# Kernel tuning notes

Hardware: AMD Instinct MI355X
Metric: run time of the kernel (lower is better)

Reference implementation:

```python
import jax, jax.numpy as jnp
import numpy as np

DN = ('NCHW', 'OIHW', 'NCHW')

def _conv(x, w, padding):
    return jax.lax.conv_general_dilated(
        x, w, window_strides=(1, 1), padding=padding,
        dimension_numbers=DN)

def setup_inputs() -> dict:
    key = jax.random.key(0)
    k1, k2, k3, k4, k5 = jax.random.split(key, 5)
    nf = 40
    x = jax.random.normal(k1, (16, nf, 256, 256), dtype=jnp.float32)
    # PyTorch conv default init scale ~ 1/sqrt(fan_in)
    w2 = jax.random.normal(k2, (nf, nf, 1, 1), dtype=jnp.float32) / np.sqrt(nf)
    b2 = jax.random.normal(k3, (nf,), dtype=jnp.float32) * 0.01
    w3 = jax.random.normal(k4, (nf, nf, 3, 3), dtype=jnp.float32) / np.sqrt(nf * 9)
    w4 = jax.random.normal(k5, (nf, nf, 3, 3), dtype=jnp.float32) / np.sqrt(nf * 9)
    return {"x": x, "w2": w2, "b2": b2, "w3": w3, "w4": w4}

def reference(x, w2, b2, w3, w4):
    # k2: 1x1 conv + bias, then sigmoid gate (pixel attention)
    y = _conv(x, w2, padding='VALID') + b2[None, :, None, None]
    y = jax.nn.sigmoid(y)
    # k3: 3x3 conv (pad 1, no bias), gated elementwise
    out = _conv(x, w3, padding=((1, 1), (1, 1))) * y
    # k4: 3x3 conv (pad 1, no bias)
    out = _conv(out, w4, padding=((1, 1), (1, 1)))
    return out
```

## Files before the change

kernel.cpp:

```cpp
#include <hip/hip_runtime.h>
#include <hip/hip_bf16.h>

typedef __bf16 bf16;
typedef __bf16 bf16x2 __attribute__((ext_vector_type(2)));
typedef __bf16 bf16x4 __attribute__((ext_vector_type(4)));
typedef __bf16 bf16x8 __attribute__((ext_vector_type(8)));
typedef float f32x4 __attribute__((ext_vector_type(4)));

#define NF 40
#define HW 256
#define KPAD 384
#define MPAD 48

#define ZROW_ELEM_OFF (2 * MPAD * KPAD + MPAD * 64)
#define GATED_ELEM_OFF 40960
#define IMG_ELEMS ((size_t)16 * HW * HW * NF)
#define XT_ELEM_OFF (GATED_ELEM_OFF + IMG_ELEMS)
#define WS_FULL  ((GATED_ELEM_OFF + 2 * IMG_ELEMS) * 2)

#define PLANE ((size_t)HW * HW * 8)
#define IMGSTR ((size_t)HW * HW * NF)

#define SRW 34
#define SRH 10
#define SRU 340
#define SGS 2720
#define SNU 1700
#define SBUF 14336

__device__ __forceinline__ void gload_lds16(const bf16* g, bf16* l) {
  __builtin_amdgcn_global_load_lds(
      (const __attribute__((address_space(1))) void*)g,
      (__attribute__((address_space(3))) void*)l, 16, 0, 0);
}

__global__ void prep_weights(const float* __restrict__ w2,
                             const float* __restrict__ w3,
                             const float* __restrict__ w4,
                             bf16* __restrict__ ws) {
  int i = blockIdx.x * 256 + threadIdx.x;
  const int T = MPAD * KPAD;
  if (i < T) {
    int co = i / KPAD, k = i % KPAD;
    float v3 = 0.f, v4 = 0.f;
    if (co < NF && k < 360) {
      int tap = k / NF, ci = k - tap * NF;
      int ky = tap / 3, kx = tap - ky * 3;
      int idx = ((co * NF + ci) * 3 + ky) * 3 + kx;
      v3 = w3[idx];
      v4 = w4[idx];
    }
    ws[i] = (bf16)v3;
    ws[T + i] = (bf16)v4;
  }
  if (i < MPAD * 64) {
    int co = i / 64, ci = i - co * 64;
    float v = 0.f;
    if (co < NF && ci < NF) v = w2[co * NF + ci];
    ws[2 * T + i] = (bf16)v;
  }
  if (i < 1024) ws[ZROW_ELEM_OFF + i] = (bf16)0.f;
}

__global__ __launch_bounds__(256, 8)
void transpose_nhwc(const float* __restrict__ x, bf16* __restrict__ xT) {
  __shared__ bf16 xs[5 * 2056];
  const int tid = threadIdx.x;
  const int row = blockIdx.x;
  const int n   = blockIdx.y;
  const size_t nb = (size_t)n * NF * HW * HW + (size_t)row * HW;

#pragma unroll
  for (int cc = 0; cc < 10; ++cc) {
    bf16x4 v;
#pragma unroll
    for (int j = 0; j < 4; ++j)
      v[j] = (bf16)x[nb + (size_t)(cc * 4 + j) * HW * HW + tid];
    *(bf16x4*)&xs[(cc >> 1) * 2056 + tid * 8 + (cc & 1) * 4] = v;
  }
  __syncthreads();

  const size_t ob = ((size_t)n * HW * HW + (size_t)row * HW) * NF;
#pragma unroll
  for (int k = 0; k < 10; ++k) {
    int u = tid + k * 256;
    int px = u / 10, c4 = u - px * 10;
    bf16x4 v = *(const bf16x4*)&xs[(c4 >> 1) * 2056 + px * 8 + (c4 & 1) * 4];
    *(bf16x4*)&xT[ob + (size_t)u * 4] = v;
  }
}

__global__ __launch_bounds__(256, 2)
void k1_sweep(const bf16* __restrict__ xT, const float* __restrict__ b2,
              const bf16* __restrict__ ws, bf16* __restrict__ gated) {
  __shared__ bf16 xs[2][SBUF];

  const int tid  = threadIdx.x;
  const int lane = tid & 63;
  const int wid  = tid >> 6;
  const int l15  = lane & 15;
  const int lk   = lane >> 4;
  const int n    = blockIdx.z;
  const int X0   = blockIdx.x * 32;
  const int Yb   = blockIdx.y * 64;

  const bf16* W3A  = ws;
  const bf16* W2A  = ws + 2 * MPAD * KPAD;
  const bf16* zrow = ws + ZROW_ELEM_OFF;
  const bf16* bn   = xT + (size_t)n * IMGSTR;

  int gp3[12];
#pragma unroll
  for (int kk = 0; kk < 12; ++kk) {
    int k0 = kk * 32 + lk * 8;
    int kc = (k0 < 360) ? k0 : 0;
    int tap = kc / NF, ci0 = kc - tap * NF;
    int ky = tap / 3, kx = tap - ky * 3;
    gp3[kk] = (ci0 >> 3) * SGS + (ky * SRW + kx) * 8;
  }
  int gctr[2];
#pragma unroll
  for (int kk = 0; kk < 2; ++kk) {
    int k0 = kk * 32 + lk * 8;
    int ci0 = (k0 < NF) ? k0 : 0;
    gctr[kk] = (ci0 >> 3) * SGS + (SRW + 1) * 8;
  }
  int pb[4];
#pragma unroll
  for (int q = 0; q < 4; ++q) {
    int prow = wid * 2 + (q >> 1);
    int pcol = (q & 1) * 16 + l15;
    pb[q] = (prow * SRW + pcol) * 8;
  }
  float b2v[3][4];
#pragma unroll
  for (int mt = 0; mt < 3; ++mt)
#pragma unroll
    for (int r = 0; r < 4; ++r) {
      int co = mt * 16 + lk * 4 + r;
      b2v[mt][r] = (co < NF) ? b2[co] : 0.f;
    }
  bf16x8 a2[2][3];
#pragma unroll
  for (int kk = 0; kk < 2; ++kk)
#pragma unroll
    for (int mt = 0; mt < 3; ++mt)
      a2[kk][mt] = *(const bf16x8*)&W2A[(mt * 16 + l15) * 64 + kk * 32 + lk * 8];

  int uc8[7], ur[7], ugx[7], uld[7];
  bool uok[7];
#pragma unroll
  for (int it = 0; it < 7; ++it) {
    int u0 = it * 256 + wid * 64;
    int u  = u0 + lane;
    int c   = u / SRU;
    int rem = u - c * SRU;
    int r   = rem / SRW;
    int p   = rem - r * SRW;
    int gx  = X0 - 1 + p;
    uok[it] = (u < SNU) && ((unsigned)gx < HW);
    uc8[it] = (c << 3);
    ur[it]  = r;
    ugx[it] = ((unsigned)gx < HW) ? gx : 0;
    uld[it] = u0 * 8;
  }

  {
    int ys = Yb - 1;
#pragma unroll
    for (int it = 0; it < 7; ++it) {
      int gy = ys + ur[it];
      bool ok = uok[it] && ((unsigned)gy < HW);
      const bf16* src = ok ? (bn + (size_t)(gy * HW + ugx[it]) * NF + uc8[it]) : zrow;
      gload_lds16(src, &xs[0][uld[it]]);
    }
  }
  __syncthreads();

  for (int s = 0; s < 8; ++s) {
    const bf16* buf = xs[s & 1];

    if (s < 7) {
      int ys = Yb + (s + 1) * 8 - 1;
      bf16* nbuf = xs[(s & 1) ^ 1];
#pragma unroll
      for (int it = 0; it < 7; ++it) {
        int gy = ys + ur[it];
        bool ok = uok[it] && ((unsigned)gy < HW);
        const bf16* src = ok ? (bn + (size_t)(gy * HW + ugx[it]) * NF + uc8[it]) : zrow;
        gload_lds16(src, &nbuf[uld[it]]);
      }
    }

    bf16x4 gv[4][3];
    {
      f32x4 g[4][3];
#pragma unroll
      for (int q = 0; q < 4; ++q)
#pragma unroll
        for (int mt = 0; mt < 3; ++mt) g[q][mt] = f32x4{0, 0, 0, 0};
#pragma unroll
      for (int kk = 0; kk < 2; ++kk)
#pragma unroll
        for (int q = 0; q < 4; ++q) {
          bf16x8 b = *(const bf16x8*)&buf[gctr[kk] + pb[q]];
#pragma unroll
          for (int mt = 0; mt < 3; ++mt)
            g[q][mt] = __builtin_amdgcn_mfma_f32_16x16x32_bf16(a2[kk][mt], b, g[q][mt], 0, 0, 0);
        }
#pragma unroll
      for (int q = 0; q < 4; ++q)
#pragma unroll
        for (int mt = 0; mt < 3; ++mt)
#pragma unroll
          for (int r = 0; r < 4; ++r)
            gv[q][mt][r] = (bf16)(1.f / (1.f + __expf(-(g[q][mt][r] + b2v[mt][r]))));
    }

    f32x4 f[4][3];
#pragma unroll
    for (int q = 0; q < 4; ++q)
#pragma unroll
      for (int mt = 0; mt < 3; ++mt) f[q][mt] = f32x4{0, 0, 0, 0};

#pragma unroll
    for (int kk = 0; kk < 12; ++kk) {
      bf16x8 a[3];
#pragma unroll
      for (int mt = 0; mt < 3; ++mt)
        a[mt] = *(const bf16x8*)&W3A[(mt * 16 + l15) * KPAD + kk * 32 + lk * 8];
#pragma unroll
      for (int q = 0; q < 4; ++q) {
        bf16x8 b = *(const bf16x8*)&buf[gp3[kk] + pb[q]];
#pragma unroll
        for (int mt = 0; mt < 3; ++mt)
          f[q][mt] = __builtin_amdgcn_mfma_f32_16x16x32_bf16(a[mt], b, f[q][mt], 0, 0, 0);
      }
    }

#pragma unroll
    for (int q = 0; q < 4; ++q) {
      int prow = wid * 2 + (q >> 1);
      int pcol = (q & 1) * 16 + l15;
      size_t pix8 = ((size_t)(Yb + s * 8 + prow) * HW + (X0 + pcol)) * 8;
#pragma unroll
      for (int mt = 0; mt < 3; ++mt) {
        int co0 = mt * 16 + lk * 4;
        if (co0 < NF) {
          int cg = co0 >> 3;
          bf16x4 ov;
#pragma unroll
          for (int r = 0; r < 4; ++r)
            ov[r] = (bf16)(f[q][mt][r] * (float)gv[q][mt][r]);
          *(bf16x4*)&gated[(size_t)n * IMGSTR + (size_t)cg * PLANE + pix8 + (co0 & 7)] = ov;
        }
      }
    }

    __syncthreads();
  }
}

__global__ __launch_bounds__(256, 2)
void k2_sweep(const bf16* __restrict__ gated, const bf16* __restrict__ ws,
              float* __restrict__ out) {
  __shared__ bf16 xs[2][SBUF];

  const int tid  = threadIdx.x;
  const int lane = tid & 63;
  const int wid  = tid >> 6;
  const int l15  = lane & 15;
  const int lk   = lane >> 4;
  const int n    = blockIdx.z;
  const int X0   = blockIdx.x * 32;
  const int Yb   = blockIdx.y * 64;

  const bf16* W4A  = ws + MPAD * KPAD;
  const bf16* zrow = ws + ZROW_ELEM_OFF;
  const bf16* bn   = gated + (size_t)n * IMGSTR;

  int gp4[12];
#pragma unroll
  for (int kk = 0; kk < 12; ++kk) {
    int k0 = kk * 32 + lk * 8;
    int kc = (k0 < 360) ? k0 : 0;
    int tap = kc / NF, ci0 = kc - tap * NF;
    int ky = tap / 3, kx = tap - ky * 3;
    gp4[kk] = (ci0 >> 3) * SGS + (ky * SRW + kx) * 8;
  }
  int pb[4];
#pragma unroll
  for (int q = 0; q < 4; ++q) {
    int prow = wid * 2 + (q >> 1);
    int pcol = (q & 1) * 16 + l15;
    pb[q] = (prow * SRW + pcol) * 8;
  }

  int ucp[7], ur[7], ugx[7], uld[7];
  bool uok[7];
#pragma unroll
  for (int it = 0; it < 7; ++it) {
    int u0 = it * 256 + wid * 64;
    int u  = u0 + lane;
    int c   = u / SRU;
    int rem = u - c * SRU;
    int r   = rem / SRW;
    int p   = rem - r * SRW;
    int gx  = X0 - 1 + p;
    uok[it] = (u < SNU) && ((unsigned)gx < HW);
    ucp[it] = (c < 5) ? c : 0;
    ur[it]  = r;
    ugx[it] = ((unsigned)gx < HW) ? gx : 0;
    uld[it] = u0 * 8;
  }

  {
    int ys = Yb - 1;
#pragma unroll
    for (int it = 0; it < 7; ++it) {
      int gy = ys + ur[it];
      bool ok = uok[it] && ((unsigned)gy < HW);
      const bf16* src = ok ? (bn + (size_t)ucp[it] * PLANE + (size_t)(gy * HW + ugx[it]) * 8) : zrow;
      gload_lds16(src, &xs[0][uld[it]]);
    }
  }
  __syncthreads();

  float* on = out + (size_t)n * NF * HW * HW;

  for (int s = 0; s < 8; ++s) {
    const bf16* buf = xs[s & 1];

    if (s < 7) {
      int ys = Yb + (s + 1) * 8 - 1;
      bf16* nbuf = xs[(s & 1) ^ 1];
#pragma unroll
      for (int it = 0; it < 7; ++it) {
        int gy = ys + ur[it];
        bool ok = uok[it] && ((unsigned)gy < HW);
        const bf16* src = ok ? (bn + (size_t)ucp[it] * PLANE + (size_t)(gy * HW + ugx[it]) * 8) : zrow;
        gload_lds16(src, &nbuf[uld[it]]);
      }
    }

    f32x4 f[4][3];
#pragma unroll
    for (int q = 0; q < 4; ++q)
#pragma unroll
      for (int mt = 0; mt < 3; ++mt) f[q][mt] = f32x4{0, 0, 0, 0};

#pragma unroll
    for (int kk = 0; kk < 12; ++kk) {
      bf16x8 a[3];
#pragma unroll
      for (int mt = 0; mt < 3; ++mt)
        a[mt] = *(const bf16x8*)&W4A[(mt * 16 + l15) * KPAD + kk * 32 + lk * 8];
#pragma unroll
      for (int q = 0; q < 4; ++q) {
        bf16x8 b = *(const bf16x8*)&buf[gp4[kk] + pb[q]];
#pragma unroll
        for (int mt = 0; mt < 3; ++mt)
          f[q][mt] = __builtin_amdgcn_mfma_f32_16x16x32_bf16(a[mt], b, f[q][mt], 0, 0, 0);
      }
    }

#pragma unroll
    for (int q = 0; q < 4; ++q) {
      int prow = wid * 2 + (q >> 1);
      int pcol = (q & 1) * 16 + l15;
      float* orow = on + (size_t)(Yb + s * 8 + prow) * HW + (X0 + pcol);
#pragma unroll
      for (int mt = 0; mt < 3; ++mt)
#pragma unroll
        for (int r = 0; r < 4; ++r) {
          int co = mt * 16 + lk * 4 + r;
          if (co < NF)
            orow[(size_t)co * HW * HW] = f[q][mt][r];
        }
    }

    __syncthreads();
  }
}

#define K1_RW 18
__global__ __launch_bounds__(512, 6)
void k1_gate_nchw(const float* __restrict__ x, const float* __restrict__ b2,
                  const bf16* __restrict__ ws, bf16* __restrict__ gated) {
  __shared__ bf16 xs[K1_RW * K1_RW * NF];

  const int tid  = threadIdx.x;
  const int lane = tid & 63;
  const int wid  = tid >> 6;
  const int l15  = lane & 15;
  const int lk   = lane >> 4;
  const int n    = blockIdx.z;
  const int X0   = blockIdx.x * 16;
  const int Y0   = blockIdx.y * 16;

  const bf16* W3A = ws;
  const bf16* W2A = ws + 2 * MPAD * KPAD;

  const float* xn = x + (size_t)n * NF * HW * HW;
  for (int i = tid; i < K1_RW * K1_RW * NF / 2; i += 512) {
    int cih = i / (K1_RW * K1_RW);
    int rem = i - cih * (K1_RW * K1_RW);
    int ci  = cih * 2;
    int yy  = rem / K1_RW, xx = rem - yy * K1_RW;
    int gy  = Y0 - 1 + yy, gx = X0 - 1 + xx;
    float v0 = 0.f, v1 = 0.f;
    if ((unsigned)gy < HW && (unsigned)gx < HW) {
      const float* p = xn + (size_t)ci * HW * HW + gy * HW + gx;
      v0 = p[0];
      v1 = p[HW * HW];
    }
    bf16x2 pr; pr[0] = (bf16)v0; pr[1] = (bf16)v1;
    *(bf16x2*)&xs[rem * NF + ci] = pr;
  }

  int off3[12];
#pragma unroll
  for (int kk = 0; kk < 12; ++kk) {
    int k0 = kk * 32 + lk * 8;
    int kc = (k0 < 360) ? k0 : 0;
    int tap = kc / NF, ci0 = kc - tap * NF;
    int ky = tap / 3, kx = tap - ky * 3;
    off3[kk] = (ky * K1_RW + kx) * NF + ci0;
  }
  int pb[2];
#pragma unroll
  for (int t2 = 0; t2 < 2; ++t2) {
    int pix = (wid * 2 + t2) * 16 + l15;
    int py = pix >> 4, px = pix & 15;
    pb[t2] = (py * K1_RW + px) * NF;
  }
  float b2v[3][4];
#pragma unroll
  for (int mt = 0; mt < 3; ++mt)
#pragma unroll
    for (int r = 0; r < 4; ++r) {
      int co = mt * 16 + lk * 4 + r;
      b2v[mt][r] = (co < NF) ? b2[co] : 0.f;
    }

  __syncthreads();

  bf16x4 gv[2][3];
  {
    f32x4 g[2][3];
#pragma unroll
    for (int t2 = 0; t2 < 2; ++t2)
#pragma unroll
      for (int mt = 0; mt < 3; ++mt) g[t2][mt] = f32x4{0, 0, 0, 0};
#pragma unroll
    for (int kk = 0; kk < 2; ++kk) {
      int k0 = kk * 32 + lk * 8;
      int goff = (K1_RW + 1) * NF + ((k0 < NF) ? k0 : 0);
      bf16x8 a[3];
#pragma unroll
      for (int mt = 0; mt < 3; ++mt)
        a[mt] = *(const bf16x8*)&W2A[(mt * 16 + l15) * 64 + k0];
#pragma unroll
      for (int t2 = 0; t2 < 2; ++t2) {
        bf16x8 b = *(const bf16x8*)&xs[pb[t2] + goff];
#pragma unroll
        for (int mt = 0; mt < 3; ++mt)
          g[t2][mt] = __builtin_amdgcn_mfma_f32_16x16x32_bf16(a[mt], b, g[t2][mt], 0, 0, 0);
      }
    }
#pragma unroll
    for (int t2 = 0; t2 < 2; ++t2)
#pragma unroll
      for (int mt = 0; mt < 3; ++mt)
#pragma unroll
        for (int r = 0; r < 4; ++r)
          gv[t2][mt][r] = (bf16)(1.f / (1.f + __expf(-(g[t2][mt][r] + b2v[mt][r]))));
  }

  f32x4 facc[2][3];
#pragma unroll
  for (int t2 = 0; t2 < 2; ++t2)
#pragma unroll
    for (int mt = 0; mt < 3; ++mt) facc[t2][mt] = f32x4{0, 0, 0, 0};

#pragma unroll
  for (int kk = 0; kk < 12; ++kk) {
    bf16x8 a[3];
#pragma unroll
    for (int mt = 0; mt < 3; ++mt)
      a[mt] = *(const bf16x8*)&W3A[(mt * 16 + l15) * KPAD + kk * 32 + lk * 8];
#pragma unroll
    for (int t2 = 0; t2 < 2; ++t2) {
      bf16x8 b = *(const bf16x8*)&xs[pb[t2] + off3[kk]];
#pragma unroll
      for (int mt = 0; mt < 3; ++mt)
        facc[t2][mt] = __builtin_amdgcn_mfma_f32_16x16x32_bf16(a[mt], b, facc[t2][mt], 0, 0, 0);
    }
  }

#pragma unroll
  for (int t2 = 0; t2 < 2; ++t2) {
    int pix = (wid * 2 + t2) * 16 + l15;
    int py = pix >> 4, px = pix & 15;
    size_t pix8 = ((size_t)(Y0 + py) * HW + (X0 + px)) * 8;
#pragma unroll
    for (int mt = 0; mt < 3; ++mt) {
      int co0 = mt * 16 + lk * 4;
      if (co0 < NF) {
        int cg = co0 >> 3;
        bf16x4 ov;
#pragma unroll
        for (int r = 0; r < 4; ++r)
          ov[r] = (bf16)(facc[t2][mt][r] * (float)gv[t2][mt][r]);
        *(bf16x4*)&gated[(size_t)n * IMGSTR + (size_t)cg * PLANE + pix8 + (co0 & 7)] = ov;
      }
    }
  }
}

extern "C" void kernel_launch(void* const* d_in, const int* in_sizes, int n_in,
                              void* d_out, int out_size, void* d_ws, size_t ws_size,
                              hipStream_t stream) {
  const float* x  = (const float*)d_in[0];
  const float* w2 = (const float*)d_in[1];
  const float* b2 = (const float*)d_in[2];
  const float* w3 = (const float*)d_in[3];
  const float* w4 = (const float*)d_in[4];
  float* out = (float*)d_out;
  bf16* ws   = (bf16*)d_ws;

  hipLaunchKernelGGL(prep_weights, dim3(72), dim3(256), 0, stream, w2, w3, w4, ws);

  bf16* gated = ws + GATED_ELEM_OFF;
  if (ws_size >= WS_FULL) {
    bf16* xT = ws + XT_ELEM_OFF;
    hipLaunchKernelGGL(transpose_nhwc, dim3(256, 16), dim3(256), 0, stream, x, xT);
    hipLaunchKernelGGL(k1_sweep, dim3(8, 4, 16), dim3(256), 0, stream,
                       xT, b2, ws, gated);
  } else {
    hipLaunchKernelGGL(k1_gate_nchw, dim3(16, 16, 16), dim3(512), 0, stream,
                       x, b2, ws, gated);
  }
  hipLaunchKernelGGL(k2_sweep, dim3(8, 4, 16), dim3(256), 0, stream,
                     gated, ws, out);
}
```

Baseline: 285.4 us.

## Relax per-step barriers to partial vmcnt waits, precompute load pointers, raise MFMA priority

Both sweep kernels end each row step with an explicit s_waitcnt vmcnt(N) plus s_barrier instead of __syncthreads. The intent is that the prefetch loads into LDS must finish, but the global stores just issued can stay in flight. The per-iteration prefetch address math is replaced by pointers computed once and advanced by a fixed stride, with a special case for the bottom boundary tile. The MFMA loops are wrapped in s_setprio to favour the compute waves. Correctness now depends on the counted number of stores per thread and on in-order vmcnt accounting.

```diff
diff --git a/kernel.cpp b/kernel.cpp
--- a/kernel.cpp
+++ b/kernel.cpp
@@ -22,7 +22,6 @@
 #define IMGSTR ((size_t)HW * HW * NF)
 
 #define SRW 34
-#define SRH 10
 #define SRU 340
 #define SGS 2720
 #define SNU 1700
@@ -33,6 +32,9 @@
       (const __attribute__((address_space(1))) void*)g,
       (__attribute__((address_space(3))) void*)l, 16, 0, 0);
 }
+
+#define BARRIER_VM(N)                                                        \
+  asm volatile("s_waitcnt vmcnt(" #N ") lgkmcnt(0)\n\ts_barrier" ::: "memory")
 
 __global__ void prep_weights(const float* __restrict__ w2,
                              const float* __restrict__ w3,
@@ -103,6 +105,7 @@
   const int n    = blockIdx.z;
   const int X0   = blockIdx.x * 32;
   const int Yb   = blockIdx.y * 64;
+  const bool lasty = (Yb == HW - 64);
 
   const bf16* W3A  = ws;
   const bf16* W2A  = ws + 2 * MPAD * KPAD;
@@ -127,11 +130,8 @@
   }
   int pb[4];
 #pragma unroll
-  for (int q = 0; q < 4; ++q) {
-    int prow = wid * 2 + (q >> 1);
-    int pcol = (q & 1) * 16 + l15;
-    pb[q] = (prow * SRW + pcol) * 8;
-  }
+  for (int q = 0; q < 4; ++q)
+    pb[q] = ((wid * 2 + (q >> 1)) * SRW + (q & 1) * 16 + l15) * 8;
   float b2v[3][4];
 #pragma unroll
   for (int mt = 0; mt < 3; ++mt)
@@ -147,7 +147,7 @@
     for (int mt = 0; mt < 3; ++mt)
       a2[kk][mt] = *(const bf16x8*)&W2A[(mt * 16 + l15) * 64 + kk * 32 + lk * 8];
 
-  int uc8[7], ur[7], ugx[7], uld[7];
+  int ur[7], ugx[7], uc8[7], uld[7];
   bool uok[7];
 #pragma unroll
   for (int it = 0; it < 7; ++it) {
@@ -159,11 +159,18 @@
     int p   = rem - r * SRW;
     int gx  = X0 - 1 + p;
     uok[it] = (u < SNU) && ((unsigned)gx < HW);
-    uc8[it] = (c << 3);
     ur[it]  = r;
     ugx[it] = ((unsigned)gx < HW) ? gx : 0;
+    uc8[it] = (c << 3);
     uld[it] = u0 * 8;
   }
+
+  const bf16* P[7];
+#pragma unroll
+  for (int it = 0; it < 7; ++it)
+    P[it] = uok[it] ? (bn + (size_t)((Yb + 7 + ur[it]) * HW + ugx[it]) * NF + uc8[it])
+                    : zrow;
+  const size_t PSTEP = (size_t)8 * HW * NF;
 
   {
     int ys = Yb - 1;
@@ -175,22 +182,32 @@
       gload_lds16(src, &xs[0][uld[it]]);
     }
   }
-  __syncthreads();
+  asm volatile("s_waitcnt vmcnt(0) lgkmcnt(0)\n\ts_barrier" ::: "memory");
+
+  bf16* gbase = gated + (size_t)n * IMGSTR;
+  size_t e0 = ((size_t)(Yb + wid * 2) * HW + X0 + l15) * 8;
+  const size_t ESTEP = (size_t)8 * HW * 8;
 
   for (int s = 0; s < 8; ++s) {
     const bf16* buf = xs[s & 1];
 
     if (s < 7) {
-      int ys = Yb + (s + 1) * 8 - 1;
       bf16* nbuf = xs[(s & 1) ^ 1];
-#pragma unroll
-      for (int it = 0; it < 7; ++it) {
-        int gy = ys + ur[it];
-        bool ok = uok[it] && ((unsigned)gy < HW);
-        const bf16* src = ok ? (bn + (size_t)(gy * HW + ugx[it]) * NF + uc8[it]) : zrow;
-        gload_lds16(src, &nbuf[uld[it]]);
-      }
-    }
+      if (lasty && s == 6) {
+#pragma unroll
+        for (int it = 0; it < 7; ++it) {
+          bool ok = uok[it] && (ur[it] < 9);
+          gload_lds16(ok ? P[it] : zrow, &nbuf[uld[it]]);
+        }
+      } else {
+#pragma unroll
+        for (int it = 0; it < 7; ++it) {
+          gload_lds16(P[it], &nbuf[uld[it]]);
+          P[it] += uok[it] ? PSTEP : 0;
+        }
+      }
+    }
+    asm volatile("" ::: "memory");
 
     bf16x4 gv[4][3];
     {
@@ -223,6 +240,7 @@
 #pragma unroll
       for (int mt = 0; mt < 3; ++mt) f[q][mt] = f32x4{0, 0, 0, 0};
 
+    __builtin_amdgcn_s_setprio(1);
 #pragma unroll
     for (int kk = 0; kk < 12; ++kk) {
       bf16x8 a[3];
@@ -237,12 +255,11 @@
           f[q][mt] = __builtin_amdgcn_mfma_f32_16x16x32_bf16(a[mt], b, f[q][mt], 0, 0, 0);
       }
     }
+    __builtin_amdgcn_s_setprio(0);
 
 #pragma unroll
     for (int q = 0; q < 4; ++q) {
-      int prow = wid * 2 + (q >> 1);
-      int pcol = (q & 1) * 16 + l15;
-      size_t pix8 = ((size_t)(Yb + s * 8 + prow) * HW + (X0 + pcol)) * 8;
+      size_t pix8 = e0 + (size_t)(((q >> 1) * HW + (q & 1) * 16) * 8);
 #pragma unroll
       for (int mt = 0; mt < 3; ++mt) {
         int co0 = mt * 16 + lk * 4;
@@ -252,12 +269,13 @@
 #pragma unroll
           for (int r = 0; r < 4; ++r)
             ov[r] = (bf16)(f[q][mt][r] * (float)gv[q][mt][r]);
-          *(bf16x4*)&gated[(size_t)n * IMGSTR + (size_t)cg * PLANE + pix8 + (co0 & 7)] = ov;
-        }
-      }
-    }
-
-    __syncthreads();
+          *(bf16x4*)&gbase[(size_t)cg * PLANE + pix8 + (co0 & 7)] = ov;
+        }
+      }
+    }
+    e0 += ESTEP;
+
+    BARRIER_VM(8);
   }
 }
 
@@ -274,6 +292,7 @@
   const int n    = blockIdx.z;
   const int X0   = blockIdx.x * 32;
   const int Yb   = blockIdx.y * 64;
+  const bool lasty = (Yb == HW - 64);
 
   const bf16* W4A  = ws + MPAD * KPAD;
   const bf16* zrow = ws + ZROW_ELEM_OFF;
@@ -290,13 +309,10 @@
   }
   int pb[4];
 #pragma unroll
-  for (int q = 0; q < 4; ++q) {
-    int prow = wid * 2 + (q >> 1);
-    int pcol = (q & 1) * 16 + l15;
-    pb[q] = (prow * SRW + pcol) * 8;
-  }
-
-  int ucp[7], ur[7], ugx[7], uld[7];
+  for (int q = 0; q < 4; ++q)
+    pb[q] = ((wid * 2 + (q >> 1)) * SRW + (q & 1) * 16 + l15) * 8;
+
+  int ur[7], ugx[7], ucp[7], uld[7];
   bool uok[7];
 #pragma unroll
   for (int it = 0; it < 7; ++it) {
@@ -308,11 +324,19 @@
     int p   = rem - r * SRW;
     int gx  = X0 - 1 + p;
     uok[it] = (u < SNU) && ((unsigned)gx < HW);
-    ucp[it] = (c < 5) ? c : 0;
     ur[it]  = r;
     ugx[it] = ((unsigned)gx < HW) ? gx : 0;
+    ucp[it] = (c < 5) ? c : 0;
     uld[it] = u0 * 8;
   }
+
+  const bf16* P[7];
+#pragma unroll
+  for (int it = 0; it < 7; ++it)
+    P[it] = uok[it] ? (bn + (size_t)ucp[it] * PLANE +
+                       (size_t)((Yb + 7 + ur[it]) * HW + ugx[it]) * 8)
+                    : zrow;
+  const size_t PSTEP = (size_t)8 * HW * 8;
 
   {
     int ys = Yb - 1;
@@ -320,28 +344,37 @@
     for (int it = 0; it < 7; ++it) {
       int gy = ys + ur[it];
       bool ok = uok[it] && ((unsigned)gy < HW);
-      const bf16* src = ok ? (bn + (size_t)ucp[it] * PLANE + (size_t)(gy * HW + ugx[it]) * 8) : zrow;
+      const bf16* src = ok ? (bn + (size_t)ucp[it] * PLANE + (size_t)(gy * HW + ugx[it]) * 8)
+                           : zrow;
       gload_lds16(src, &xs[0][uld[it]]);
     }
   }
-  __syncthreads();
+  asm volatile("s_waitcnt vmcnt(0) lgkmcnt(0)\n\ts_barrier" ::: "memory");
 
   float* on = out + (size_t)n * NF * HW * HW;
+  size_t o0 = (size_t)(Yb + wid * 2) * HW + X0 + l15;
+  const size_t OSTEP = (size_t)8 * HW;
 
   for (int s = 0; s < 8; ++s) {
     const bf16* buf = xs[s & 1];
 
     if (s < 7) {
-      int ys = Yb + (s + 1) * 8 - 1;
       bf16* nbuf = xs[(s & 1) ^ 1];
-#pragma unroll
-      for (int it = 0; it < 7; ++it) {
-        int gy = ys + ur[it];
-        bool ok = uok[it] && ((unsigned)gy < HW);
-        const bf16* src = ok ? (bn + (size_t)ucp[it] * PLANE + (size_t)(gy * HW + ugx[it]) * 8) : zrow;
-        gload_lds16(src, &nbuf[uld[it]]);
-      }
-    }
+      if (lasty && s == 6) {
+#pragma unroll
+        for (int it = 0; it < 7; ++it) {
+          bool ok = uok[it] && (ur[it] < 9);
+          gload_lds16(ok ? P[it] : zrow, &nbuf[uld[it]]);
+        }
+      } else {
+#pragma unroll
+        for (int it = 0; it < 7; ++it) {
+          gload_lds16(P[it], &nbuf[uld[it]]);
+          P[it] += uok[it] ? PSTEP : 0;
+        }
+      }
+    }
+    asm volatile("" ::: "memory");
 
     f32x4 f[4][3];
 #pragma unroll
@@ -349,6 +382,7 @@
 #pragma unroll
       for (int mt = 0; mt < 3; ++mt) f[q][mt] = f32x4{0, 0, 0, 0};
 
+    __builtin_amdgcn_s_setprio(1);
 #pragma unroll
     for (int kk = 0; kk < 12; ++kk) {
       bf16x8 a[3];
@@ -363,12 +397,11 @@
           f[q][mt] = __builtin_amdgcn_mfma_f32_16x16x32_bf16(a[mt], b, f[q][mt], 0, 0, 0);
       }
     }
+    __builtin_amdgcn_s_setprio(0);
 
 #pragma unroll
     for (int q = 0; q < 4; ++q) {
-      int prow = wid * 2 + (q >> 1);
-      int pcol = (q & 1) * 16 + l15;
-      float* orow = on + (size_t)(Yb + s * 8 + prow) * HW + (X0 + pcol);
+      float* orow = on + o0 + ((q >> 1) * HW + (q & 1) * 16);
 #pragma unroll
       for (int mt = 0; mt < 3; ++mt)
 #pragma unroll
@@ -378,8 +411,9 @@
             orow[(size_t)co * HW * HW] = f[q][mt][r];
         }
     }
-
-    __syncthreads();
+    o0 += OSTEP;
+
+    BARRIER_VM(32);
   }
 }
 
```

After: 256.0 us. 1.11x faster.
